# Optimization experiments

Measured on AMD Instinct MI355X. Metric: run time of the kernel, lower is better.

## Reference

```python
import jax, jax.numpy as jnp
import numpy as np
import math

D_MODEL = 1024
N_HEADS = 16
D_K = D_MODEL // N_HEADS
B, S = 4, 2048


def setup_inputs() -> dict:
    key = jax.random.key(0)
    ks = jax.random.split(key, 11)
    sc = 1.0 / math.sqrt(D_MODEL)
    inp = {
        'q': jax.random.normal(ks[0], (B, S, D_MODEL), jnp.float32),
        'k': jax.random.normal(ks[1], (B, S, D_MODEL), jnp.float32),
        'v': jax.random.normal(ks[2], (B, S, D_MODEL), jnp.float32),
        'mask': jnp.tril(jnp.ones((S, S), jnp.int32))[None, None],  # [1,1,S,S] causal
        'wq': jax.random.normal(ks[3], (D_MODEL, D_MODEL), jnp.float32) * sc,
        'bq': jnp.zeros((D_MODEL,), jnp.float32),
        'wk': jax.random.normal(ks[4], (D_MODEL, D_MODEL), jnp.float32) * sc,
        'bk': jnp.zeros((D_MODEL,), jnp.float32),
        'wv': jax.random.normal(ks[5], (D_MODEL, D_MODEL), jnp.float32) * sc,
        'bv': jnp.zeros((D_MODEL,), jnp.float32),
        'wo': jax.random.normal(ks[6], (D_MODEL, D_MODEL), jnp.float32) * sc,
        'bo': jnp.zeros((D_MODEL,), jnp.float32),
    }
    return inp


def reference(q, k, v, mask, wq, bq, wk, bk, wv, bv, wo, bo):
    b = q.shape[0]
    # projections: [B,S,D] -> [B,H,S,d_k]
    def split_heads(x):
        return x.reshape(b, -1, N_HEADS, D_K).transpose(0, 2, 1, 3)
    qh = split_heads(q @ wq + bq)
    kh = split_heads(k @ wk + bk)
    vh = split_heads(v @ wv + bv)
    # scores: [B,H,S,S]
    scores = jnp.einsum('bhqd,bhkd->bhqk', qh, kh) / math.sqrt(D_K)
    scores = jnp.where(mask == 0, jnp.float32(-1e9), scores)
    attn = jax.nn.softmax(scores, axis=-1)
    # dropout is identity in eval mode (deterministic reference)
    ctx = jnp.einsum('bhqk,bhkd->bhqd', attn, vh)
    ctx = ctx.transpose(0, 2, 1, 3).reshape(b, -1, D_MODEL)
    return ctx @ wo + bo
```

## Files before the change

kernel.cpp:

```cpp
#include <hip/hip_runtime.h>
#include <hip/hip_bf16.h>

#define D_MODEL 1024
#define N_HEADS 16
#define DK 64
#define SEQ 2048
#define BATCH 4

typedef __attribute__((ext_vector_type(4))) float   f32v4;
typedef __attribute__((ext_vector_type(16))) float  f32v16;
typedef __attribute__((ext_vector_type(8))) __bf16  bf16x8;
typedef __attribute__((ext_vector_type(8))) unsigned short u16v8;
typedef __attribute__((ext_vector_type(4))) unsigned short u16v4;
typedef __attribute__((ext_vector_type(4))) unsigned int   u32v4;

#define QSCALE 0.18033688011112042f
#define SMBIAS 12.0f

__device__ __forceinline__ int swz(int byte) {
    return byte ^ (((byte >> 7) & 7) << 4);
}

__device__ __forceinline__ unsigned short bfb(float f) {
    return __builtin_bit_cast(unsigned short, (__bf16)f);
}
__device__ __forceinline__ float bff(unsigned short u) {
    return (float)__builtin_bit_cast(__bf16, u);
}

__device__ __forceinline__ f32v4 mfma16(bf16x8 a, bf16x8 b, f32v4 c) {
    return __builtin_amdgcn_mfma_f32_16x16x32_bf16(a, b, c, 0, 0, 0);
}
__device__ __forceinline__ f32v16 mfma32(bf16x8 a, bf16x8 b, f32v16 c) {
    return __builtin_amdgcn_mfma_f32_32x32x16_bf16(a, b, c, 0, 0, 0);
}

#define GL2LDS16(gp, lp) \
    __builtin_amdgcn_global_load_lds((__attribute__((address_space(1))) const void*)(gp), \
                                     (__attribute__((address_space(3))) void*)(lp), 16, 0, 0)

#define VMWAIT(N) asm volatile("s_waitcnt vmcnt(" #N ")" ::: "memory")
#define LGKM0()   asm volatile("s_waitcnt lgkmcnt(0)" ::: "memory")

__global__ __launch_bounds__(256) void wtrans_kernel(const float* wq, const float* wk,
                                                     const float* wv, const float* wo,
                                                     unsigned short* wt) {
    __shared__ unsigned short ts[64][65];
    int bid = blockIdx.x;
    int mat = bid >> 8;
    int tile = bid & 255;
    int kb = (tile >> 4) * 64;
    int nb = (tile & 15) * 64;
    const float* W = (mat == 0) ? wq : (mat == 1) ? wk : (mat == 2) ? wv : wo;
    unsigned short* out = wt + (size_t)mat * D_MODEL * D_MODEL;
    int t = threadIdx.x;
#pragma unroll
    for (int p = 0; p < 4; ++p) {
        int row = p * 16 + (t >> 4);
        int c0 = (t & 15) * 4;
        f32v4 v = *(const f32v4*)(W + (size_t)(kb + row) * D_MODEL + nb + c0);
#pragma unroll
        for (int j = 0; j < 4; ++j) ts[row][c0 + j] = bfb(v[j]);
    }
    __syncthreads();
#pragma unroll
    for (int p = 0; p < 2; ++p) {
        int n = p * 32 + (t >> 3);
        int k0 = (t & 7) * 8;
        u16v8 o;
#pragma unroll
        for (int j = 0; j < 8; ++j) o[j] = ts[k0 + j][n];
        *(u16v8*)(out + (size_t)(nb + n) * D_MODEL + kb + k0) = o;
    }
}

__global__ __launch_bounds__(256, 2) void qkv_kernel(const float* __restrict__ qin,
                                                     const float* __restrict__ kin,
                                                     const float* __restrict__ vin,
                                                     const unsigned short* __restrict__ WT,
                                                     const float* __restrict__ bq,
                                                     const float* __restrict__ bk,
                                                     const float* __restrict__ bv,
                                                     unsigned short* __restrict__ Qh,
                                                     unsigned short* __restrict__ Kh,
                                                     unsigned short* __restrict__ Vtp) {
    __shared__ unsigned short lds[2][(128 + 128) * 64];
    int bid0 = blockIdx.x;
    int mat = bid0 >> 9;
    int bidl = bid0 & 511;
    const float* Af = (mat == 0) ? qin : (mat == 1) ? kin : vin;
    const unsigned short* Wt = WT + (size_t)mat * D_MODEL * D_MODEL;
    const float* bias = (mat == 0) ? bq : (mat == 1) ? bk : bv;
    bool vmode = (mat == 2);
    float osc = (mat == 0) ? QSCALE : 1.0f;

    int xcd = bidl & 7, blki = bidl >> 3;
    int mb = (xcd * 8 + (blki >> 3)) * 128;
    int nb = (blki & 7) * 128;
    int tid = threadIdx.x;
    int lane = tid & 63, wid = tid >> 6;
    int l15 = lane & 15, g = lane >> 4;
    int r7 = lane >> 3, slot = lane & 7;
    int wr = wid >> 1, wc = wid & 1;
    int ssrc = (slot ^ r7) * 8;

    f32v4 acc[4][4] = {};

    char* p0 = (char*)lds[0];
    char* p1 = (char*)lds[1];

    int arow = tid >> 4;
    int acol = (tid & 15) * 4;
    f32v4 a_stg[8];

    auto stage_issue = [&](char* buf, int k0) {
#pragma unroll
        for (int j = 0; j < 8; ++j)
            a_stg[j] = *(const f32v4*)(Af + (size_t)(mb + j * 16 + arow) * D_MODEL + k0 + acol);
#pragma unroll
        for (int ii = 0; ii < 4; ++ii) {
            int c = ii * 4 + wid;
            GL2LDS16(Wt + (size_t)(nb + c * 8 + r7) * D_MODEL + k0 + ssrc, buf + 16384 + c * 1024);
        }
    };
    auto stage_write = [&](char* buf) {
#pragma unroll
        for (int j = 0; j < 8; ++j) {
            u16v4 o;
#pragma unroll
            for (int e = 0; e < 4; ++e) o[e] = bfb(a_stg[j][e]);
            int row = j * 16 + arow;
            *(u16v4*)(buf + swz(row * 128 + (tid & 15) * 8)) = o;
        }
    };
    auto fragA = [&](char* buf, int row, int kk) -> bf16x8 {
        int sl = (kk * 4 + g) ^ (row & 7);
        return *(bf16x8*)(buf + row * 128 + sl * 16);
    };
    auto fragB = [&](char* buf, int row, int kk) -> bf16x8 {
        int sl = (kk * 4 + g) ^ (row & 7);
        return *(bf16x8*)(buf + 16384 + row * 128 + sl * 16);
    };

    stage_issue(p0, 0);
    stage_write(p0);
    VMWAIT(0);
    LGKM0();
    __builtin_amdgcn_s_barrier();
    __builtin_amdgcn_sched_barrier(0);

    for (int t = 0; t < 16; ++t) {
        if (t < 15) stage_issue(p1, (t + 1) * 64);
#pragma unroll
        for (int kk = 0; kk < 2; ++kk) {
            bf16x8 fa[4], fb[4];
            if (!vmode) {
#pragma unroll
                for (int mt = 0; mt < 4; ++mt) fa[mt] = fragA(p0, wr * 64 + mt * 16 + l15, kk);
#pragma unroll
                for (int nt = 0; nt < 4; ++nt) fb[nt] = fragB(p0, wc * 64 + nt * 16 + l15, kk);
            } else {
#pragma unroll
                for (int xx = 0; xx < 4; ++xx) fa[xx] = fragB(p0, wc * 64 + xx * 16 + l15, kk);
#pragma unroll
                for (int yy = 0; yy < 4; ++yy) fb[yy] = fragA(p0, wr * 64 + yy * 16 + l15, kk);
            }
            __builtin_amdgcn_s_setprio(1);
#pragma unroll
            for (int a = 0; a < 4; ++a)
#pragma unroll
                for (int b = 0; b < 4; ++b)
                    acc[a][b] = mfma16(fa[a], fb[b], acc[a][b]);
            __builtin_amdgcn_s_setprio(0);
        }
        if (t < 15) {
            stage_write(p1);
            VMWAIT(0);
            LGKM0();
            __builtin_amdgcn_s_barrier();
            __builtin_amdgcn_sched_barrier(0);
            char* tp = p0; p0 = p1; p1 = tp;
        }
    }

    if (!vmode) {
        unsigned short* out = (mat == 0) ? Qh : Kh;
#pragma unroll
        for (int nt = 0; nt < 4; ++nt) {
            int n = nb + wc * 64 + nt * 16 + l15;
            float bvv = bias[n];
#pragma unroll
            for (int mt = 0; mt < 4; ++mt) {
#pragma unroll
                for (int r = 0; r < 4; ++r) {
                    int m = mb + wr * 64 + mt * 16 + 4 * g + r;
                    float val = (acc[mt][nt][r] + bvv) * osc;
                    int bb = m >> 11, ss = m & 2047, hh = n >> 6, dd = n & 63;
                    out[(((size_t)(bb * N_HEADS + hh)) * SEQ + ss) * DK + dd] = bfb(val);
                }
            }
        }
    } else {
#pragma unroll
        for (int xx = 0; xx < 4; ++xx) {
#pragma unroll
            for (int r = 0; r < 4; ++r) {
                int n = nb + wc * 64 + xx * 16 + 4 * g + r;
                float bvv = bias[n];
                int hh = n >> 6, dd = n & 63;
#pragma unroll
                for (int yy = 0; yy < 4; ++yy) {
                    int tok = mb + wr * 64 + yy * 16 + l15;
                    int bb = tok >> 11, ss = tok & 2047;
                    float val = acc[xx][yy][r] + bvv;
                    Vtp[((size_t)(bb * N_HEADS + hh) * DK + dd) * SEQ + ss] = bfb(val);
                }
            }
        }
    }
}

__global__ __launch_bounds__(256, 2) void gemmo_kernel(const unsigned short* __restrict__ A,
                                                       const unsigned short* __restrict__ Wt,
                                                       const float* __restrict__ bias, float* Cptr) {
    __shared__ unsigned short lds[2][(128 + 128) * 64];
    int bid0 = blockIdx.x;
    int xcd = bid0 & 7, blki = bid0 >> 3;
    int mb = (xcd * 8 + (blki >> 3)) * 128;
    int nb = (blki & 7) * 128;
    int tid = threadIdx.x;
    int lane = tid & 63, wid = tid >> 6;
    int l15 = lane & 15, g = lane >> 4;
    int r7 = lane >> 3, slot = lane & 7;
    int wr = wid >> 1, wc = wid & 1;
    int ssrc = (slot ^ r7) * 8;

    f32v4 acc[4][4] = {};
    char* p0 = (char*)lds[0];
    char* p1 = (char*)lds[1];

    auto stage = [&](char* buf, int k0) {
#pragma unroll
        for (int ii = 0; ii < 4; ++ii) {
            int c = ii * 4 + wid;
            GL2LDS16(A + (size_t)(mb + c * 8 + r7) * D_MODEL + k0 + ssrc, buf + c * 1024);
        }
#pragma unroll
        for (int ii = 0; ii < 4; ++ii) {
            int c = ii * 4 + wid;
            GL2LDS16(Wt + (size_t)(nb + c * 8 + r7) * D_MODEL + k0 + ssrc, buf + 16384 + c * 1024);
        }
    };
    auto fragA = [&](char* buf, int row, int kk) -> bf16x8 {
        int sl = (kk * 4 + g) ^ (row & 7);
        return *(bf16x8*)(buf + row * 128 + sl * 16);
    };
    auto fragB = [&](char* buf, int row, int kk) -> bf16x8 {
        int sl = (kk * 4 + g) ^ (row & 7);
        return *(bf16x8*)(buf + 16384 + row * 128 + sl * 16);
    };

    stage(p0, 0);
    VMWAIT(0);
    __builtin_amdgcn_s_barrier();
    __builtin_amdgcn_sched_barrier(0);

    for (int t = 0; t < 16; ++t) {
        if (t < 15) stage(p1, (t + 1) * 64);
#pragma unroll
        for (int kk = 0; kk < 2; ++kk) {
            bf16x8 fa[4], fb[4];
#pragma unroll
            for (int mt = 0; mt < 4; ++mt) fa[mt] = fragA(p0, wr * 64 + mt * 16 + l15, kk);
#pragma unroll
            for (int nt = 0; nt < 4; ++nt) fb[nt] = fragB(p0, wc * 64 + nt * 16 + l15, kk);
            __builtin_amdgcn_s_setprio(1);
#pragma unroll
            for (int a = 0; a < 4; ++a)
#pragma unroll
                for (int b = 0; b < 4; ++b)
                    acc[a][b] = mfma16(fa[a], fb[b], acc[a][b]);
            __builtin_amdgcn_s_setprio(0);
        }
        if (t < 15) {
            VMWAIT(0);
            __builtin_amdgcn_s_barrier();
            __builtin_amdgcn_sched_barrier(0);
            char* tp = p0; p0 = p1; p1 = tp;
        }
    }

#pragma unroll
    for (int nt = 0; nt < 4; ++nt) {
        int n = nb + wc * 64 + nt * 16 + l15;
        float bv = bias[n];
#pragma unroll
        for (int mt = 0; mt < 4; ++mt) {
#pragma unroll
            for (int r = 0; r < 4; ++r) {
                int m = mb + wr * 64 + mt * 16 + 4 * g + r;
                Cptr[(size_t)m * D_MODEL + n] = acc[mt][nt][r] + bv;
            }
        }
    }
}

__global__ __launch_bounds__(256, 4) void attn_kernel(const unsigned short* Qh, const unsigned short* Kh,
                                                      const unsigned short* Vt, unsigned short* ctxp) {
    __shared__ unsigned short k_lds[2][64 * 64];
    __shared__ unsigned short v_lds[2][64 * 64];
    int bid = blockIdx.x;
    int jq = bid >> 8, x = (bid >> 6) & 3;
    int tile = (jq == 0) ? (15 - x) : (jq == 1) ? (8 + x) : (jq == 2) ? (7 - x) : x;
    int bh = bid & 63;
    int bb = bh >> 4, hh = bh & 15;
    int tid = threadIdx.x;
    int wid = tid >> 6, lane = tid & 63;
    int l31 = lane & 31, hi = lane >> 5;
    int qw0 = tile * 128 + wid * 32;
    int qg = qw0 + l31;
    const unsigned short* Qb = Qh + (size_t)bh * SEQ * DK;
    const unsigned short* Kb = Kh + (size_t)bh * SEQ * DK;
    const unsigned short* Vb = Vt + (size_t)bh * DK * SEQ;

    bf16x8 qf[4];
#pragma unroll
    for (int ks = 0; ks < 4; ++ks)
        qf[ks] = *(const bf16x8*)(Qb + (size_t)qg * DK + ks * 16 + hi * 8);

    f32v16 o0 = {}, o1 = {};
    float lsum = 0.f;
    int n_kt = 2 * tile + 2;

    const int klane = 16 * (lane ^ (lane >> 3));
    const int vlane = 16 * ((lane & 7) ^ (lane >> 3));
    auto stage = [&](int bufi, int kg) {
        const char* kb0 = (const char*)(Kb + (size_t)kg * DK);
        const char* vb0 = (const char*)Vb + (size_t)kg * 2;
#pragma unroll
        for (int jj = 0; jj < 2; ++jj) {
            int base = wid * 2048 + jj * 1024;
            GL2LDS16(kb0 + base + klane, (char*)k_lds[bufi] + base);
            GL2LDS16(vb0 + (size_t)(wid * 16 + jj * 8 + (lane >> 3)) * (SEQ * 2) + vlane,
                     (char*)v_lds[bufi] + base);
        }
    };

#define PACK2(a, b) (((unsigned)bfb(b) << 16) | (unsigned)bfb(a))
#define PVSTEP(tt, r0, ks, vl)                                                          \
    {                                                                                   \
        unsigned x0 = PACK2(tt[r0 + 0], tt[r0 + 1]);                                    \
        unsigned x1 = PACK2(tt[r0 + 2], tt[r0 + 3]);                                    \
        unsigned x2 = PACK2(tt[r0 + 4], tt[r0 + 5]);                                    \
        unsigned x3 = PACK2(tt[r0 + 6], tt[r0 + 7]);                                    \
        asm volatile("v_permlane32_swap_b32 %0, %1" : "+v"(x0), "+v"(x2));              \
        asm volatile("v_permlane32_swap_b32 %0, %1" : "+v"(x1), "+v"(x3));              \
        u32v4 w;                                                                        \
        w[0] = x0;  w[1] = x1;  w[2] = x2;  w[3] = x3;                                  \
        bf16x8 paf = __builtin_bit_cast(bf16x8, w);                                     \
        bf16x8 vf0 = *(bf16x8*)((char*)(vl) + swz(l31 * 128 + ks * 32 + hi * 16));      \
        bf16x8 vf1 = *(bf16x8*)((char*)(vl) + swz((32 + l31) * 128 + ks * 32 + hi * 16)); \
        o0 = mfma32(paf, vf0, o0);                                                      \
        o1 = mfma32(paf, vf1, o1);                                                      \
    }

    auto compute_tile = [&](int ktb, const unsigned short* kl, const unsigned short* vl) {
        if (ktb > qw0 + 31) return;
        f32v16 t0 = {}, t1 = {};
        __builtin_amdgcn_s_setprio(1);
#pragma unroll
        for (int ks = 0; ks < 4; ++ks) {
            bf16x8 kf0 = *(bf16x8*)((char*)kl + swz(l31 * 128 + ks * 32 + hi * 16));
            bf16x8 kf1 = *(bf16x8*)((char*)kl + swz((32 + l31) * 128 + ks * 32 + hi * 16));
            t0 = mfma32(kf0, qf[ks], t0);
            t1 = mfma32(kf1, qf[ks], t1);
        }
        __builtin_amdgcn_s_setprio(0);
        if (ktb + 63 > qw0) {
#pragma unroll
            for (int r = 0; r < 16; ++r) {
                int off = (r & 3) + 8 * (r >> 2) + 4 * hi;
                if (ktb + off > qg) t0[r] = -1e30f;
                if (ktb + 32 + off > qg) t1[r] = -1e30f;
            }
        }
#pragma unroll
        for (int r = 0; r < 16; ++r) {
            t0[r] = __builtin_amdgcn_exp2f(t0[r] - SMBIAS);
            t1[r] = __builtin_amdgcn_exp2f(t1[r] - SMBIAS);
            lsum += t0[r] + t1[r];
        }
        __builtin_amdgcn_s_setprio(1);
        PVSTEP(t0, 0, 0, vl)
        PVSTEP(t0, 8, 1, vl)
        PVSTEP(t1, 0, 2, vl)
        PVSTEP(t1, 8, 3, vl)
        __builtin_amdgcn_s_setprio(0);
    };

    stage(0, 0);
    __syncthreads();
    int buf = 0;
    for (int kt = 0; kt < n_kt; ++kt) {
        if (kt + 1 < n_kt) stage(buf ^ 1, (kt + 1) * 64);
        compute_tile(kt * 64, k_lds[buf], v_lds[buf]);
        __syncthreads();
        buf ^= 1;
    }

    float lt = lsum + __shfl_xor(lsum, 32);
    float rinv = 1.f / lt;
#pragma unroll
    for (int r = 0; r < 16; ++r) {
        int off = (r & 3) + 8 * (r >> 2) + 4 * hi;
        float rr = __shfl(rinv, off);
        int qq = qw0 + off;
        size_t base = ((size_t)(bb * SEQ + qq)) * D_MODEL + hh * DK;
        ctxp[base + l31] = bfb(o0[r] * rr);
        ctxp[base + 32 + l31] = bfb(o1[r] * rr);
    }
#undef PVSTEP
#undef PACK2
}

extern "C" void kernel_launch(void* const* d_in, const int* in_sizes, int n_in,
                              void* d_out, int out_size, void* d_ws, size_t ws_size,
                              hipStream_t stream) {
    const float* q  = (const float*)d_in[0];
    const float* k  = (const float*)d_in[1];
    const float* v  = (const float*)d_in[2];
    const float* wq = (const float*)d_in[4];
    const float* bq = (const float*)d_in[5];
    const float* wk = (const float*)d_in[6];
    const float* bk = (const float*)d_in[7];
    const float* wv = (const float*)d_in[8];
    const float* bv = (const float*)d_in[9];
    const float* wo = (const float*)d_in[10];
    const float* bo = (const float*)d_in[11];

    unsigned short* ws  = (unsigned short*)d_ws;
    const size_t M8 = (size_t)8 * 1024 * 1024;
    unsigned short* Qh = ws;
    unsigned short* Kh = ws + M8;
    unsigned short* Vt = ws + 2 * M8;
    unsigned short* X  = ws + 3 * M8;
    unsigned short* WT = ws + 4 * M8;
    const size_t MM = (size_t)D_MODEL * D_MODEL;

    wtrans_kernel<<<dim3(1024), dim3(256), 0, stream>>>(wq, wk, wv, wo, WT);
    qkv_kernel<<<dim3(1536), dim3(256), 0, stream>>>(q, k, v, WT, bq, bk, bv, Qh, Kh, Vt);
    attn_kernel<<<dim3(1024), dim3(256), 0, stream>>>(Qh, Kh, Vt, X);
    gemmo_kernel<<<dim3(512), dim3(256), 0, stream>>>(X, WT + 3 * MM, bo, (float*)d_out);
}
```

Baseline: 153.0 us.

## Triple-buffer weight tiles in QKV GEMM to prefetch two stages ahead

Splits the shared-memory staging into separate A (activation) and B (weight) buffers. B is triple-buffered and loaded by direct global-to-LDS DMA two k-steps ahead, so the full vector-memory wait before each barrier can be dropped. This aims to hide global-load latency behind the MFMA loop. In exchange it uses more LDS (about 80KB per block), which may pressure the two-blocks-per-CU occupancy target. Correctness now relies on in-order vmcnt completion, implied by the compiler's wait for the A-register loads.

```diff
diff --git a/kernel.cpp b/kernel.cpp
--- a/kernel.cpp
+++ b/kernel.cpp
@@ -84,7 +84,8 @@
                                                      unsigned short* __restrict__ Qh,
                                                      unsigned short* __restrict__ Kh,
                                                      unsigned short* __restrict__ Vtp) {
-    __shared__ unsigned short lds[2][(128 + 128) * 64];
+    __shared__ unsigned short lds_a[2][128 * 64];
+    __shared__ unsigned short lds_b[3][128 * 64];
     int bid0 = blockIdx.x;
     int mat = bid0 >> 9;
     int bidl = bid0 & 511;
@@ -106,24 +107,23 @@
 
     f32v4 acc[4][4] = {};
 
-    char* p0 = (char*)lds[0];
-    char* p1 = (char*)lds[1];
-
     int arow = tid >> 4;
     int acol = (tid & 15) * 4;
     f32v4 a_stg[8];
 
-    auto stage_issue = [&](char* buf, int k0) {
+    auto issueA = [&](int k0) {
 #pragma unroll
         for (int j = 0; j < 8; ++j)
             a_stg[j] = *(const f32v4*)(Af + (size_t)(mb + j * 16 + arow) * D_MODEL + k0 + acol);
+    };
+    auto dmaB = [&](char* buf, int k0) {
 #pragma unroll
         for (int ii = 0; ii < 4; ++ii) {
             int c = ii * 4 + wid;
-            GL2LDS16(Wt + (size_t)(nb + c * 8 + r7) * D_MODEL + k0 + ssrc, buf + 16384 + c * 1024);
-        }
-    };
-    auto stage_write = [&](char* buf) {
+            GL2LDS16(Wt + (size_t)(nb + c * 8 + r7) * D_MODEL + k0 + ssrc, buf + c * 1024);
+        }
+    };
+    auto writeA = [&](char* buf) {
 #pragma unroll
         for (int j = 0; j < 8; ++j) {
             u16v4 o;
@@ -139,31 +139,36 @@
     };
     auto fragB = [&](char* buf, int row, int kk) -> bf16x8 {
         int sl = (kk * 4 + g) ^ (row & 7);
-        return *(bf16x8*)(buf + 16384 + row * 128 + sl * 16);
-    };
-
-    stage_issue(p0, 0);
-    stage_write(p0);
+        return *(bf16x8*)(buf + row * 128 + sl * 16);
+    };
+
+    issueA(0);
+    dmaB((char*)lds_b[0], 0);
+    dmaB((char*)lds_b[1], 64);
+    writeA((char*)lds_a[0]);
     VMWAIT(0);
     LGKM0();
     __builtin_amdgcn_s_barrier();
     __builtin_amdgcn_sched_barrier(0);
 
     for (int t = 0; t < 16; ++t) {
-        if (t < 15) stage_issue(p1, (t + 1) * 64);
+        if (t < 15) issueA((t + 1) * 64);
+        if (t + 2 < 16) dmaB((char*)lds_b[(t + 2) % 3], (t + 2) * 64);
+        char* pa = (char*)lds_a[t & 1];
+        char* pb = (char*)lds_b[t % 3];
 #pragma unroll
         for (int kk = 0; kk < 2; ++kk) {
             bf16x8 fa[4], fb[4];
             if (!vmode) {
 #pragma unroll
-                for (int mt = 0; mt < 4; ++mt) fa[mt] = fragA(p0, wr * 64 + mt * 16 + l15, kk);
-#pragma unroll
-                for (int nt = 0; nt < 4; ++nt) fb[nt] = fragB(p0, wc * 64 + nt * 16 + l15, kk);
+                for (int mt = 0; mt < 4; ++mt) fa[mt] = fragA(pa, wr * 64 + mt * 16 + l15, kk);
+#pragma unroll
+                for (int nt = 0; nt < 4; ++nt) fb[nt] = fragB(pb, wc * 64 + nt * 16 + l15, kk);
             } else {
 #pragma unroll
-                for (int xx = 0; xx < 4; ++xx) fa[xx] = fragB(p0, wc * 64 + xx * 16 + l15, kk);
-#pragma unroll
-                for (int yy = 0; yy < 4; ++yy) fb[yy] = fragA(p0, wr * 64 + yy * 16 + l15, kk);
+                for (int xx = 0; xx < 4; ++xx) fa[xx] = fragB(pb, wc * 64 + xx * 16 + l15, kk);
+#pragma unroll
+                for (int yy = 0; yy < 4; ++yy) fb[yy] = fragA(pa, wr * 64 + yy * 16 + l15, kk);
             }
             __builtin_amdgcn_s_setprio(1);
 #pragma unroll
@@ -174,12 +179,10 @@
             __builtin_amdgcn_s_setprio(0);
         }
         if (t < 15) {
-            stage_write(p1);
-            VMWAIT(0);
+            writeA((char*)lds_a[(t + 1) & 1]);
             LGKM0();
             __builtin_amdgcn_s_barrier();
             __builtin_amdgcn_sched_barrier(0);
-            char* tp = p0; p0 = p1; p1 = tp;
         }
     }
 
```

After: 164.7 us. 7.6% more time.
